# Performance work log

Hardware: AMD Instinct MI355X
Metric: run time of the kernel (lower is better)

The kernel has to match this reference:

```python
import jax, jax.numpy as jnp
import numpy as np

B, S, H = 1, 4096, 2048
NH, NKV, HD = 8, 4, 256
I = 8192
EPS = 1e-6
THETA = 10000.0
WINDOW = 4096  # hardcoded sliding window for even layer_idx
LAYER_IDX = 0


def rms_norm(x, w):
    v = jnp.mean(jnp.square(x), axis=-1, keepdims=True)
    return x * jax.lax.rsqrt(v + EPS) * w


def rotate_half(x):
    h = x.shape[-1] // 2
    return jnp.concatenate([-x[..., h:], x[..., :h]], axis=-1)


def apply_rope(q, k, positions):
    # q: [B,S,NH,HD], k: [B,S,NKV,HD], positions: [B,S]
    inv_freq = 1.0 / (THETA ** (jnp.arange(0, HD, 2, dtype=jnp.float32) / HD))
    freqs = positions.astype(jnp.float32)[..., None] * inv_freq  # [B,S,HD/2]
    emb = jnp.concatenate([freqs, freqs], axis=-1)               # [B,S,HD]
    cos = jnp.cos(emb)[:, :, None, :]
    sin = jnp.sin(emb)[:, :, None, :]
    q = q * cos + rotate_half(q) * sin
    k = k * cos + rotate_half(k) * sin
    return q, k


def forward(hidden_states, q_w, k_w, v_w, o_w, gate_w, up_w, down_w, ln1_w, ln2_w,
            attention_mask, position_ids):
    # ---- input RMSNorm + attention ----
    residual = hidden_states
    x = rms_norm(hidden_states, ln1_w)

    q = (x @ q_w).reshape(B, S, NH, HD)
    k = (x @ k_w).reshape(B, S, NKV, HD)
    v = (x @ v_w).reshape(B, S, NKV, HD)
    q, k = apply_rope(q, k, position_ids)

    # GQA: repeat kv heads to match query heads
    groups = NH // NKV
    k = jnp.repeat(k, groups, axis=2)  # [B,S,NH,HD]
    v = jnp.repeat(v, groups, axis=2)

    # masks: padding mask AND causal AND (even layer) local window of WINDOW
    row = jnp.arange(S)[:, None]
    col = jnp.arange(S)[None, :]
    causal = col <= row                                   # [S,S]
    combined = causal[None, None] & (attention_mask[:, None, None, :] > 0)
    if LAYER_IDX % 2 == 0:
        keep = ~(col <= row - WINDOW)                     # mask out keys older than WINDOW
        combined = combined & keep[None, None]
    neg = jnp.finfo(jnp.float32).min
    bias = jnp.where(combined, 0.0, neg).astype(jnp.float32)  # [B,1,S,S]

    scale = HD ** -0.5
    scores = jnp.einsum('bqhd,bkhd->bhqk', q, k) * scale + bias
    probs = jax.nn.softmax(scores, axis=-1)
    attn = jnp.einsum('bhqk,bkhd->bqhd', probs, v).reshape(B, S, NH * HD)
    attn_out = attn @ o_w

    hidden_states = residual + attn_out

    # ---- post-attention RMSNorm + gated-GeLU MLP ----
    residual = hidden_states
    x = rms_norm(hidden_states, ln2_w)
    mlp = (jax.nn.gelu(x @ gate_w, approximate=True) * (x @ up_w)) @ down_w
    return residual + mlp


def setup_inputs() -> dict:
    key = jax.random.key(0)
    ks = jax.random.split(key, 9)
    std = 0.02
    n = lambda k, shp: jax.random.normal(k, shp, dtype=jnp.float32) * std
    return {
        'hidden_states': jax.random.normal(ks[0], (B, S, H), dtype=jnp.float32),
        'q_w': n(ks[1], (H, NH * HD)),
        'k_w': n(ks[2], (H, NKV * HD)),
        'v_w': n(ks[3], (H, NKV * HD)),
        'o_w': n(ks[4], (NH * HD, H)),
        'gate_w': n(ks[5], (H, I)),
        'up_w': n(ks[6], (H, I)),
        'down_w': n(ks[7], (I, H)),
        'ln1_w': jnp.ones((H,), jnp.float32),
        'ln2_w': jnp.ones((H,), jnp.float32),
        'attention_mask': jnp.ones((B, S), jnp.int32),
        'position_ids': jnp.broadcast_to(jnp.arange(S, dtype=jnp.int32)[None, :], (B, S)),
    }


def reference(hidden_states, q_w, k_w, v_w, o_w, gate_w, up_w, down_w, ln1_w, ln2_w,
              attention_mask, position_ids):
    return forward(hidden_states, q_w, k_w, v_w, o_w, gate_w, up_w, down_w,
                   ln1_w, ln2_w, attention_mask, position_ids)
```

## Files before the change

### kernel.cpp

```cpp
#include <hip/hip_runtime.h>
#include <hip/hip_bf16.h>
#include <math.h>

#define S_LEN 4096
#define HID   2048
#define NHEADS 8
#define NKVH   4
#define HDIM   256
#define FFN    8192
#define WIN    4096

typedef __bf16 bf16_t;
typedef __bf16 bf16x4 __attribute__((ext_vector_type(4)));
typedef __bf16 bf16x8 __attribute__((ext_vector_type(8)));
typedef float  floatx4 __attribute__((ext_vector_type(4)));

__device__ inline float waveReduceSum(float v) {
#pragma unroll
    for (int o = 32; o > 0; o >>= 1) v += __shfl_xor(v, o);
    return v;
}
__device__ inline float blockReduceSum(float v, float* sh) {
    int tid = threadIdx.x;
    v = waveReduceSum(v);
    if ((tid & 63) == 0) sh[tid >> 6] = v;
    __syncthreads();
    v = sh[0] + sh[1] + sh[2] + sh[3];
    __syncthreads();
    return v;
}

template <typename T>
__global__ __launch_bounds__(256) void transpose_bf16_kernel(const T* __restrict__ in,
                                                             bf16_t* __restrict__ out,
                                                             int R, int C) {
    __shared__ float tile[32][33];
    int tx = threadIdx.x & 31;
    int ty = threadIdx.x >> 5;
    int c0 = blockIdx.x * 32;
    int r0 = blockIdx.y * 32;
#pragma unroll
    for (int i = 0; i < 4; ++i)
        tile[ty + i * 8][tx] = (float)in[(long long)(r0 + ty + i * 8) * C + c0 + tx];
    __syncthreads();
#pragma unroll
    for (int i = 0; i < 4; ++i)
        out[(long long)(c0 + ty + i * 8) * R + r0 + tx] = (bf16_t)tile[tx][ty + i * 8];
}

__global__ __launch_bounds__(256) void rmsnorm_kernel(const float* __restrict__ x,
                                                      const float* __restrict__ w,
                                                      bf16_t* __restrict__ out) {
    __shared__ float sh[4];
    int row = blockIdx.x;
    const float* xr = x + (long long)row * HID;
    float v[8];
    float ss = 0.f;
#pragma unroll
    for (int i = 0; i < 8; ++i) {
        v[i] = xr[threadIdx.x + i * 256];
        ss += v[i] * v[i];
    }
    ss = blockReduceSum(ss, sh);
    float sc = rsqrtf(ss * (1.0f / HID) + 1e-6f);
#pragma unroll
    for (int i = 0; i < 8; ++i) {
        int c = threadIdx.x + i * 256;
        out[(long long)row * HID + c] = (bf16_t)(v[i] * sc * w[c]);
    }
}

__global__ __launch_bounds__(256) void rope_kernel(bf16_t* __restrict__ q,
                                                   bf16_t* __restrict__ k,
                                                   const int* __restrict__ pos_ids) {
    int s = blockIdx.x;
    float p = (float)pos_ids[s];
    for (int t = threadIdx.x; t < (NHEADS + NKVH) * (HDIM / 2); t += 256) {
        int head = t >> 7;
        int i = t & 127;
        float inv = expf(-(2.0f * (float)i / (float)HDIM) * 9.210340371976184f);
        float f = p * inv;
        float sn, cs;
        sincosf(f, &sn, &cs);
        bf16_t* base = (head < NHEADS) ? (q + (long long)s * HID + head * HDIM)
                                       : (k + (long long)s * (NKVH * HDIM) + (head - NHEADS) * HDIM);
        float a = (float)base[i];
        float b = (float)base[i + 128];
        base[i]       = (bf16_t)(a * cs - b * sn);
        base[i + 128] = (bf16_t)(b * cs + a * sn);
    }
}

__global__ __launch_bounds__(256, 2) void flash_attn_kernel(const bf16_t* __restrict__ qg,
                                                            const bf16_t* __restrict__ kg,
                                                            const bf16_t* __restrict__ vTg,
                                                            bf16_t* __restrict__ op0,
                                                            bf16_t* __restrict__ opb123,
                                                            float* __restrict__ mlb,
                                                            const int* __restrict__ amask) {
    __shared__ bf16_t sK[64 * 256];
    __shared__ bf16_t sV[256 * 64];

    const int b = blockIdx.x;
    const int h = b & 7;
    const int j = b >> 3;
    const int jq = j & 3;
    const int pidx = j >> 2;
    const int tid = threadIdx.x;
    const int lane = tid & 63;
    const int w = tid >> 6;
    const int tl = lane & 15;
    const int quad = lane >> 4;

    const bf16_t* Qh = qg + h * HDIM;
    const bf16_t* Kh = kg + (h >> 1) * HDIM;
    const bf16_t* Vh = vTg + (long long)(h >> 1) * HDIM * S_LEN;
    bf16_t* Op = (jq == 0) ? op0 : opb123 + (long long)(jq - 1) * (S_LEN * HID);
    float* mlj = mlb + (long long)jq * (NHEADS * S_LEN * 2);
    bf16_t* sP = sK + w * (32 * 72);

#pragma unroll 1
    for (int half = 0; half < 2; ++half) {
        const int qi = half ? (31 - pidx) : pidx;
        const int qr0 = qi * 128;
        const int T = 2 * qi + 2;
        const int t0 = (T * jq) >> 2;
        const int t1 = (T * (jq + 1)) >> 2;
        const int irow = qr0 + w * 32 + tl;

        bf16x8 qf[2][8];
#pragma unroll
        for (int s = 0; s < 2; ++s) {
            const bf16_t* qrow = Qh + (long long)(irow + s * 16) * HID;
#pragma unroll
            for (int ks = 0; ks < 8; ++ks)
                qf[s][ks] = *(const bf16x8*)(qrow + (ks * 4 + quad) * 8);
        }

        floatx4 oacc[2][16] = {};
        float m_i[2] = {-3e38f, -3e38f};
        float l_i[2] = {0.f, 0.f};

        for (int t = t0; t < t1; ++t) {
            const int kt = t * 64;
#pragma unroll
            for (int it = 0; it < 8; ++it) {
                int f = it * 4 + w;
                {
                    int row = (f & 3) * 16 + tl;
                    int dc = (f >> 2) * 4 + quad;
                    const bf16_t* src = Kh + (long long)(kt + row) * (NKVH * HDIM) + dc * 8;
                    __builtin_amdgcn_global_load_lds((const __attribute__((address_space(1))) void*)src,
                                                     (__attribute__((address_space(3))) void*)(sK + (it * 256 + tid) * 8),
                                                     16, 0, 0);
                }
                {
                    int d = (f & 15) * 16 + tl;
                    int kc = (f >> 4) * 4 + quad;
                    const bf16_t* src = Vh + (long long)d * S_LEN + kt + kc * 8;
                    __builtin_amdgcn_global_load_lds((const __attribute__((address_space(1))) void*)src,
                                                     (__attribute__((address_space(3))) void*)(sV + (it * 256 + tid) * 8),
                                                     16, 0, 0);
                }
            }
            __builtin_amdgcn_s_waitcnt(0x0f70);
            __syncthreads();

            floatx4 sacc[2][4] = {};
#pragma unroll
            for (int ks = 0; ks < 8; ++ks) {
#pragma unroll
                for (int ni = 0; ni < 4; ++ni) {
                    bf16x8 kf = *(const bf16x8*)(sK + ((ks * 4 + ni) * 64 + lane) * 8);
                    sacc[0][ni] = __builtin_amdgcn_mfma_f32_16x16x32_bf16(kf, qf[0][ks], sacc[0][ni], 0, 0, 0);
                    sacc[1][ni] = __builtin_amdgcn_mfma_f32_16x16x32_bf16(kf, qf[1][ks], sacc[1][ni], 0, 0, 0);
                }
            }
            __syncthreads();

            int4 am4[4];
#pragma unroll
            for (int ni = 0; ni < 4; ++ni) am4[ni] = *(const int4*)(amask + kt + ni * 16 + quad * 4);
#pragma unroll
            for (int s = 0; s < 2; ++s) {
                const int ir = irow + s * 16;
                float sv[4][4];
                float mx = -3e38f;
#pragma unroll
                for (int ni = 0; ni < 4; ++ni) {
#pragma unroll
                    for (int r = 0; r < 4; ++r) {
                        int jk = kt + ni * 16 + quad * 4 + r;
                        int amr = (r == 0) ? am4[ni].x : (r == 1) ? am4[ni].y : (r == 2) ? am4[ni].z : am4[ni].w;
                        bool valid = (jk <= ir) && (jk > ir - WIN) && (amr > 0);
                        float x = valid ? sacc[s][ni][r] * 0.0625f : -3e38f;
                        sv[ni][r] = x;
                        mx = fmaxf(mx, x);
                    }
                }
                mx = fmaxf(mx, __shfl_xor(mx, 16));
                mx = fmaxf(mx, __shfl_xor(mx, 32));
                if (__any(mx > m_i[s])) {
                    float mnew = fmaxf(m_i[s], mx);
                    float alpha = __expf(m_i[s] - mnew);
                    m_i[s] = mnew;
                    l_i[s] *= alpha;
                    floatx4 av;
#pragma unroll
                    for (int r = 0; r < 4; ++r) av[r] = __shfl(alpha, quad * 4 + r);
#pragma unroll
                    for (int dt = 0; dt < 16; ++dt) oacc[s][dt] *= av;
                }
                float rs = 0.f;
#pragma unroll
                for (int ni = 0; ni < 4; ++ni) {
                    bf16x4 pk;
#pragma unroll
                    for (int r = 0; r < 4; ++r) {
                        float p = (sv[ni][r] > -1e37f) ? __expf(sv[ni][r] - m_i[s]) : 0.f;
                        rs += p;
                        pk[r] = (bf16_t)p;
                    }
                    *(bf16x4*)(sP + (s * 16 + tl) * 72 + ni * 16 + quad * 4) = pk;
                }
                rs += __shfl_xor(rs, 16);
                rs += __shfl_xor(rs, 32);
                l_i[s] += rs;
            }

#pragma unroll
            for (int k2 = 0; k2 < 2; ++k2) {
                bf16x8 pf0 = *(const bf16x8*)(sP + tl * 72 + k2 * 32 + quad * 8);
                bf16x8 pf1 = *(const bf16x8*)(sP + (16 + tl) * 72 + k2 * 32 + quad * 8);
#pragma unroll
                for (int dt = 0; dt < 16; ++dt) {
                    bf16x8 vf = *(const bf16x8*)(sV + ((k2 * 16 + dt) * 64 + lane) * 8);
                    oacc[0][dt] = __builtin_amdgcn_mfma_f32_16x16x32_bf16(pf0, vf, oacc[0][dt], 0, 0, 0);
                    oacc[1][dt] = __builtin_amdgcn_mfma_f32_16x16x32_bf16(pf1, vf, oacc[1][dt], 0, 0, 0);
                }
            }
            __syncthreads();
        }

#pragma unroll
        for (int s = 0; s < 2; ++s) {
            floatx4 inv;
#pragma unroll
            for (int r = 0; r < 4; ++r) {
                float lv = __shfl(l_i[s], quad * 4 + r);
                inv[r] = (lv > 0.f) ? 1.0f / lv : 0.f;
            }
#pragma unroll
            for (int dt = 0; dt < 16; ++dt) {
#pragma unroll
                for (int r = 0; r < 4; ++r) {
                    long long row = qr0 + w * 32 + s * 16 + quad * 4 + r;
                    Op[row * HID + h * HDIM + dt * 16 + tl] = (bf16_t)(oacc[s][dt][r] * inv[r]);
                }
            }
            if (quad == 0) {
                long long mi2 = ((long long)h * S_LEN + irow + s * 16) * 2;
                mlj[mi2] = m_i[s];
                mlj[mi2 + 1] = l_i[s];
            }
        }
    }
}

__global__ __launch_bounds__(256) void combine_kernel(const bf16_t* __restrict__ op0,
                                                      const bf16_t* __restrict__ opb123,
                                                      const float* __restrict__ mlb,
                                                      bf16_t* __restrict__ attnb) {
    int h = blockIdx.x;
    int row = blockIdx.y;
    int d = threadIdx.x;
    float m[4], l[4];
    float M = -3e38f;
#pragma unroll
    for (int j = 0; j < 4; ++j) {
        long long mi = (((long long)j * NHEADS + h) * S_LEN + row) * 2;
        m[j] = mlb[mi];
        l[j] = mlb[mi + 1];
        M = fmaxf(M, m[j]);
    }
    float wj[4], wsum = 0.f;
#pragma unroll
    for (int j = 0; j < 4; ++j) {
        wj[j] = (l[j] > 0.f) ? l[j] * __expf(m[j] - M) : 0.f;
        wsum += wj[j];
    }
    float inv = 1.0f / wsum;
    long long idx = (long long)row * HID + h * HDIM + d;
    float acc = wj[0] * (float)op0[idx];
#pragma unroll
    for (int j = 1; j < 4; ++j)
        acc += wj[j] * (float)opb123[(long long)(j - 1) * (S_LEN * HID) + idx];
    attnb[idx] = (bf16_t)(acc * inv);
}

template <int MODE>
__global__ __launch_bounds__(256) void gemm_kernel(const bf16_t* __restrict__ A, int lda,
                                                   const bf16_t* __restrict__ Bt, int ldb,
                                                   void* __restrict__ Cv, int ldc,
                                                   const void* __restrict__ aux, int K) {
    __shared__ bf16_t smem[2 * 128 * 64];
    bf16_t* sA = smem;
    bf16_t* sB = smem + 128 * 64;

    const int tid = threadIdx.x;
    const int n0 = blockIdx.x * 128;
    const int m0 = blockIdx.y * 128;

    const int lane = tid & 63;
    const int wid = tid >> 6;
    const int wm = (wid >> 1) * 64;
    const int wn = (wid & 1) * 64;
    const int tl = lane & 15;
    const int quad = lane >> 4;

    floatx4 acc[4][4] = {};

    for (int k0 = 0; k0 < K; k0 += 64) {
#pragma unroll
        for (int it = 0; it < 4; ++it) {
            int s = it * 256 + tid;
            int m = s >> 3;
            int sg = s & 7;
            int g = sg ^ (m & 7);
            const bf16_t* ga = A + (long long)(m0 + m) * lda + k0 + g * 8;
            __builtin_amdgcn_global_load_lds((const __attribute__((address_space(1))) void*)ga,
                                             (__attribute__((address_space(3))) void*)(sA + s * 8),
                                             16, 0, 0);
            const bf16_t* gb = Bt + (long long)(n0 + m) * ldb + k0 + g * 8;
            __builtin_amdgcn_global_load_lds((const __attribute__((address_space(1))) void*)gb,
                                             (__attribute__((address_space(3))) void*)(sB + s * 8),
                                             16, 0, 0);
        }
        __builtin_amdgcn_s_waitcnt(0x0f70);
        __syncthreads();

#pragma unroll
        for (int kk = 0; kk < 2; ++kk) {
            bf16x8 af[4], bfr[4];
#pragma unroll
            for (int mi = 0; mi < 4; ++mi) {
                int m = wm + mi * 16 + tl;
                int sg = (kk * 4 + quad) ^ (m & 7);
                af[mi] = *(const bf16x8*)(sA + m * 64 + sg * 8);
            }
#pragma unroll
            for (int ni = 0; ni < 4; ++ni) {
                int n = wn + ni * 16 + tl;
                int sg = (kk * 4 + quad) ^ (n & 7);
                bfr[ni] = *(const bf16x8*)(sB + n * 64 + sg * 8);
            }
#pragma unroll
            for (int mi = 0; mi < 4; ++mi)
#pragma unroll
                for (int ni = 0; ni < 4; ++ni)
                    acc[mi][ni] = __builtin_amdgcn_mfma_f32_16x16x32_bf16(af[mi], bfr[ni], acc[mi][ni], 0, 0, 0);
        }
        __syncthreads();
    }

#pragma unroll
    for (int mi = 0; mi < 4; ++mi) {
#pragma unroll
        for (int ni = 0; ni < 4; ++ni) {
#pragma unroll
            for (int r = 0; r < 4; ++r) {
                int gr = m0 + wm + mi * 16 + quad * 4 + r;
                int gc = n0 + wn + ni * 16 + tl;
                long long idx = (long long)gr * ldc + gc;
                float v = acc[mi][ni][r];
                if (MODE == 0) {
                    ((bf16_t*)Cv)[idx] = (bf16_t)v;
                } else if (MODE == 1) {
                    ((float*)Cv)[idx] = ((const float*)aux)[idx] + v;
                } else {
                    float g = (float)((const bf16_t*)aux)[idx];
                    float t = 0.7978845608028654f * (g + 0.044715f * g * g * g);
                    float ge = 0.5f * g * (1.0f + tanhf(t));
                    ((bf16_t*)Cv)[idx] = (bf16_t)(ge * v);
                }
            }
        }
    }
}

extern "C" void kernel_launch(void* const* d_in, const int* in_sizes, int n_in,
                              void* d_out, int out_size, void* d_ws, size_t ws_size,
                              hipStream_t stream) {
    const float* hidden = (const float*)d_in[0];
    const float* q_w    = (const float*)d_in[1];
    const float* k_w    = (const float*)d_in[2];
    const float* v_w    = (const float*)d_in[3];
    const float* o_w    = (const float*)d_in[4];
    const float* gate_w = (const float*)d_in[5];
    const float* up_w   = (const float*)d_in[6];
    const float* down_w = (const float*)d_in[7];
    const float* ln1_w  = (const float*)d_in[8];
    const float* ln2_w  = (const float*)d_in[9];
    const int* amask    = (const int*)d_in[10];
    const int* pos_ids  = (const int*)d_in[11];
    float* out = (float*)d_out;

    const size_t MB = 1ull << 20;
    char* ws = (char*)d_ws;
    bf16_t* wqT    = (bf16_t*)(ws + 0 * MB);
    bf16_t* wkT    = (bf16_t*)(ws + 8 * MB);
    bf16_t* wvT    = (bf16_t*)(ws + 12 * MB);
    bf16_t* woT    = (bf16_t*)(ws + 16 * MB);
    bf16_t* wgT    = (bf16_t*)(ws + 24 * MB);
    bf16_t* wuT    = (bf16_t*)(ws + 56 * MB);
    bf16_t* xb     = (bf16_t*)(ws + 88 * MB);
    bf16_t* qb     = (bf16_t*)(ws + 104 * MB);
    bf16_t* kb     = (bf16_t*)(ws + 120 * MB);
    bf16_t* vb     = (bf16_t*)(ws + 128 * MB);
    bf16_t* vT     = (bf16_t*)(ws + 136 * MB);
    bf16_t* op0    = (bf16_t*)(ws + 88 * MB);
    bf16_t* opb123 = (bf16_t*)(ws + 144 * MB);
    float*  mlb    = (float*) (ws + 192 * MB);
    bf16_t* attnb  = (bf16_t*)(ws + 104 * MB);
    bf16_t* xb2    = (bf16_t*)(ws + 120 * MB);
    bf16_t* wdT    = (bf16_t*)(ws + 144 * MB);
    bf16_t* gb     = (bf16_t*)(ws + 88 * MB);
    (void)ws_size; (void)in_sizes; (void)n_in; (void)out_size;

    dim3 blk(256);

    transpose_bf16_kernel<float><<<dim3(64, 64), blk, 0, stream>>>(q_w, wqT, 2048, 2048);
    transpose_bf16_kernel<float><<<dim3(32, 64), blk, 0, stream>>>(k_w, wkT, 2048, 1024);
    transpose_bf16_kernel<float><<<dim3(32, 64), blk, 0, stream>>>(v_w, wvT, 2048, 1024);
    transpose_bf16_kernel<float><<<dim3(64, 64), blk, 0, stream>>>(o_w, woT, 2048, 2048);
    transpose_bf16_kernel<float><<<dim3(256, 64), blk, 0, stream>>>(gate_w, wgT, 2048, 8192);
    transpose_bf16_kernel<float><<<dim3(256, 64), blk, 0, stream>>>(up_w, wuT, 2048, 8192);

    rmsnorm_kernel<<<dim3(S_LEN), blk, 0, stream>>>(hidden, ln1_w, xb);

    gemm_kernel<0><<<dim3(16, 32), blk, 0, stream>>>(xb, HID, wqT, HID, qb, 2048, nullptr, HID);
    gemm_kernel<0><<<dim3(8, 32), blk, 0, stream>>>(xb, HID, wkT, HID, kb, 1024, nullptr, HID);
    gemm_kernel<0><<<dim3(8, 32), blk, 0, stream>>>(xb, HID, wvT, HID, vb, 1024, nullptr, HID);

    rope_kernel<<<dim3(S_LEN), blk, 0, stream>>>(qb, kb, pos_ids);

    transpose_bf16_kernel<bf16_t><<<dim3(32, 128), blk, 0, stream>>>(vb, vT, S_LEN, 1024);

    flash_attn_kernel<<<dim3(512), blk, 0, stream>>>(qb, kb, vT, op0, opb123, mlb, amask);
    combine_kernel<<<dim3(NHEADS, S_LEN), blk, 0, stream>>>(op0, opb123, mlb, attnb);

    gemm_kernel<1><<<dim3(16, 32), blk, 0, stream>>>(attnb, 2048, woT, 2048, out, 2048, hidden, 2048);

    rmsnorm_kernel<<<dim3(S_LEN), blk, 0, stream>>>(out, ln2_w, xb2);

    transpose_bf16_kernel<float><<<dim3(64, 256), blk, 0, stream>>>(down_w, wdT, 8192, 2048);

    for (int c = 0; c < 2; ++c) {
        bf16_t* wgc = wgT + (size_t)c * 4096 * HID;
        bf16_t* wuc = wuT + (size_t)c * 4096 * HID;
        bf16_t* wdc = wdT + (size_t)c * 4096;
        gemm_kernel<0><<<dim3(32, 32), blk, 0, stream>>>(xb2, HID, wgc, HID, gb, 4096, nullptr, HID);
        gemm_kernel<2><<<dim3(32, 32), blk, 0, stream>>>(xb2, HID, wuc, HID, gb, 4096, gb, HID);
        gemm_kernel<1><<<dim3(16, 32), blk, 0, stream>>>(gb, 4096, wdc, FFN, out, 2048, out, 4096);
    }
}
```

Baseline: 1.393 ms.

## Share KV tiles across GQA head pair and double-buffer K loads in flash attention

Flash attention blocks now have 512 threads covering both query heads of a KV group, so each K/V tile loaded into LDS serves two heads. K tiles are double-buffered so the next tile's load overlaps the current tile's compute. The softmax scale is folded into the Q projection GEMM epilogue, and the causal check is skipped for tiles entirely below the diagonal. The window check is dropped because WIN equals S, so it never masks anything. LDS use grows and occupancy falls to one block per CU, and the combine kernel gains a guard against a zero weight sum.

```diff
diff --git a/kernel.cpp b/kernel.cpp
--- a/kernel.cpp
+++ b/kernel.cpp
@@ -91,42 +91,42 @@
     }
 }
 
-__global__ __launch_bounds__(256, 2) void flash_attn_kernel(const bf16_t* __restrict__ qg,
+__global__ __launch_bounds__(512, 1) void flash_attn_kernel(const bf16_t* __restrict__ qg,
                                                             const bf16_t* __restrict__ kg,
                                                             const bf16_t* __restrict__ vTg,
                                                             bf16_t* __restrict__ op0,
                                                             bf16_t* __restrict__ opb123,
                                                             float* __restrict__ mlb,
                                                             const int* __restrict__ amask) {
-    __shared__ bf16_t sK[64 * 256];
-    __shared__ bf16_t sV[256 * 64];
-
-    const int b = blockIdx.x;
-    const int h = b & 7;
-    const int j = b >> 3;
-    const int jq = j & 3;
-    const int pidx = j >> 2;
+    __shared__ bf16_t sK[2][64 * 256];
+    __shared__ bf16_t sV[64 * 256];
+    __shared__ bf16_t sPB[8 * 32 * 72];
+
+    const int kvh = blockIdx.y;
+    const int jq = blockIdx.z;
     const int tid = threadIdx.x;
     const int lane = tid & 63;
     const int w = tid >> 6;
+    const int wq = w & 3;
     const int tl = lane & 15;
     const int quad = lane >> 4;
+    const int h = kvh * 2 + (w >> 2);
 
     const bf16_t* Qh = qg + h * HDIM;
-    const bf16_t* Kh = kg + (h >> 1) * HDIM;
-    const bf16_t* Vh = vTg + (long long)(h >> 1) * HDIM * S_LEN;
+    const bf16_t* Kh = kg + kvh * HDIM;
+    const bf16_t* Vh = vTg + (long long)kvh * HDIM * S_LEN;
     bf16_t* Op = (jq == 0) ? op0 : opb123 + (long long)(jq - 1) * (S_LEN * HID);
     float* mlj = mlb + (long long)jq * (NHEADS * S_LEN * 2);
-    bf16_t* sP = sK + w * (32 * 72);
+    bf16_t* sP = sPB + w * (32 * 72);
 
 #pragma unroll 1
     for (int half = 0; half < 2; ++half) {
-        const int qi = half ? (31 - pidx) : pidx;
+        const int qi = half ? (31 - blockIdx.x) : blockIdx.x;
         const int qr0 = qi * 128;
         const int T = 2 * qi + 2;
         const int t0 = (T * jq) >> 2;
         const int t1 = (T * (jq + 1)) >> 2;
-        const int irow = qr0 + w * 32 + tl;
+        const int irow = qr0 + wq * 32 + tl;
 
         bf16x8 qf[2][8];
 #pragma unroll
@@ -141,105 +141,120 @@
         float m_i[2] = {-3e38f, -3e38f};
         float l_i[2] = {0.f, 0.f};
 
-        for (int t = t0; t < t1; ++t) {
-            const int kt = t * 64;
-#pragma unroll
-            for (int it = 0; it < 8; ++it) {
-                int f = it * 4 + w;
-                {
-                    int row = (f & 3) * 16 + tl;
-                    int dc = (f >> 2) * 4 + quad;
-                    const bf16_t* src = Kh + (long long)(kt + row) * (NKVH * HDIM) + dc * 8;
+        if (t0 < t1) {
+#pragma unroll
+            for (int it = 0; it < 4; ++it) {
+                int f = it * 8 + w;
+                const bf16_t* src = Kh + (long long)(t0 * 64 + (f & 3) * 16 + tl) * (NKVH * HDIM) + ((f >> 2) * 4 + quad) * 8;
+                __builtin_amdgcn_global_load_lds((const __attribute__((address_space(1))) void*)src,
+                                                 (__attribute__((address_space(3))) void*)(&sK[0][(it * 512 + tid) * 8]),
+                                                 16, 0, 0);
+            }
+            __syncthreads();
+            int cb = 0;
+#pragma unroll 1
+            for (int t = t0; t < t1; ++t) {
+                const int kt = t * 64;
+#pragma unroll
+                for (int it = 0; it < 4; ++it) {
+                    int f = it * 8 + w;
+                    const bf16_t* src = Vh + (long long)((f & 15) * 16 + tl) * S_LEN + kt + ((f >> 4) * 4 + quad) * 8;
                     __builtin_amdgcn_global_load_lds((const __attribute__((address_space(1))) void*)src,
-                                                     (__attribute__((address_space(3))) void*)(sK + (it * 256 + tid) * 8),
+                                                     (__attribute__((address_space(3))) void*)(&sV[(it * 512 + tid) * 8]),
                                                      16, 0, 0);
                 }
-                {
-                    int d = (f & 15) * 16 + tl;
-                    int kc = (f >> 4) * 4 + quad;
-                    const bf16_t* src = Vh + (long long)d * S_LEN + kt + kc * 8;
-                    __builtin_amdgcn_global_load_lds((const __attribute__((address_space(1))) void*)src,
-                                                     (__attribute__((address_space(3))) void*)(sV + (it * 256 + tid) * 8),
-                                                     16, 0, 0);
-                }
-            }
-            __builtin_amdgcn_s_waitcnt(0x0f70);
-            __syncthreads();
-
-            floatx4 sacc[2][4] = {};
-#pragma unroll
-            for (int ks = 0; ks < 8; ++ks) {
-#pragma unroll
-                for (int ni = 0; ni < 4; ++ni) {
-                    bf16x8 kf = *(const bf16x8*)(sK + ((ks * 4 + ni) * 64 + lane) * 8);
-                    sacc[0][ni] = __builtin_amdgcn_mfma_f32_16x16x32_bf16(kf, qf[0][ks], sacc[0][ni], 0, 0, 0);
-                    sacc[1][ni] = __builtin_amdgcn_mfma_f32_16x16x32_bf16(kf, qf[1][ks], sacc[1][ni], 0, 0, 0);
-                }
-            }
-            __syncthreads();
-
-            int4 am4[4];
-#pragma unroll
-            for (int ni = 0; ni < 4; ++ni) am4[ni] = *(const int4*)(amask + kt + ni * 16 + quad * 4);
-#pragma unroll
-            for (int s = 0; s < 2; ++s) {
-                const int ir = irow + s * 16;
-                float sv[4][4];
-                float mx = -3e38f;
-#pragma unroll
-                for (int ni = 0; ni < 4; ++ni) {
-#pragma unroll
-                    for (int r = 0; r < 4; ++r) {
-                        int jk = kt + ni * 16 + quad * 4 + r;
-                        int amr = (r == 0) ? am4[ni].x : (r == 1) ? am4[ni].y : (r == 2) ? am4[ni].z : am4[ni].w;
-                        bool valid = (jk <= ir) && (jk > ir - WIN) && (amr > 0);
-                        float x = valid ? sacc[s][ni][r] * 0.0625f : -3e38f;
-                        sv[ni][r] = x;
-                        mx = fmaxf(mx, x);
-                    }
-                }
-                mx = fmaxf(mx, __shfl_xor(mx, 16));
-                mx = fmaxf(mx, __shfl_xor(mx, 32));
-                if (__any(mx > m_i[s])) {
-                    float mnew = fmaxf(m_i[s], mx);
-                    float alpha = __expf(m_i[s] - mnew);
-                    m_i[s] = mnew;
-                    l_i[s] *= alpha;
-                    floatx4 av;
-#pragma unroll
-                    for (int r = 0; r < 4; ++r) av[r] = __shfl(alpha, quad * 4 + r);
-#pragma unroll
-                    for (int dt = 0; dt < 16; ++dt) oacc[s][dt] *= av;
-                }
-                float rs = 0.f;
-#pragma unroll
-                for (int ni = 0; ni < 4; ++ni) {
-                    bf16x4 pk;
-#pragma unroll
-                    for (int r = 0; r < 4; ++r) {
-                        float p = (sv[ni][r] > -1e37f) ? __expf(sv[ni][r] - m_i[s]) : 0.f;
-                        rs += p;
-                        pk[r] = (bf16_t)p;
-                    }
-                    *(bf16x4*)(sP + (s * 16 + tl) * 72 + ni * 16 + quad * 4) = pk;
-                }
-                rs += __shfl_xor(rs, 16);
-                rs += __shfl_xor(rs, 32);
-                l_i[s] += rs;
-            }
-
-#pragma unroll
-            for (int k2 = 0; k2 < 2; ++k2) {
-                bf16x8 pf0 = *(const bf16x8*)(sP + tl * 72 + k2 * 32 + quad * 8);
-                bf16x8 pf1 = *(const bf16x8*)(sP + (16 + tl) * 72 + k2 * 32 + quad * 8);
-#pragma unroll
-                for (int dt = 0; dt < 16; ++dt) {
-                    bf16x8 vf = *(const bf16x8*)(sV + ((k2 * 16 + dt) * 64 + lane) * 8);
-                    oacc[0][dt] = __builtin_amdgcn_mfma_f32_16x16x32_bf16(pf0, vf, oacc[0][dt], 0, 0, 0);
-                    oacc[1][dt] = __builtin_amdgcn_mfma_f32_16x16x32_bf16(pf1, vf, oacc[1][dt], 0, 0, 0);
-                }
-            }
-            __syncthreads();
+                if (t + 1 < t1) {
+#pragma unroll
+                    for (int it = 0; it < 4; ++it) {
+                        int f = it * 8 + w;
+                        const bf16_t* src = Kh + (long long)(kt + 64 + (f & 3) * 16 + tl) * (NKVH * HDIM) + ((f >> 2) * 4 + quad) * 8;
+                        __builtin_amdgcn_global_load_lds((const __attribute__((address_space(1))) void*)src,
+                                                         (__attribute__((address_space(3))) void*)(&sK[cb ^ 1][(it * 512 + tid) * 8]),
+                                                         16, 0, 0);
+                    }
+                }
+
+                const bf16_t* sKb = sK[cb];
+                floatx4 sacc[2][4] = {};
+#pragma unroll
+                for (int ks = 0; ks < 8; ++ks) {
+#pragma unroll
+                    for (int ni = 0; ni < 4; ++ni) {
+                        bf16x8 kf = *(const bf16x8*)(sKb + ((ks * 4 + ni) * 64 + lane) * 8);
+                        sacc[0][ni] = __builtin_amdgcn_mfma_f32_16x16x32_bf16(kf, qf[0][ks], sacc[0][ni], 0, 0, 0);
+                        sacc[1][ni] = __builtin_amdgcn_mfma_f32_16x16x32_bf16(kf, qf[1][ks], sacc[1][ni], 0, 0, 0);
+                    }
+                }
+                __syncthreads();
+
+                int4 am4[4];
+#pragma unroll
+                for (int ni = 0; ni < 4; ++ni) am4[ni] = *(const int4*)(amask + kt + ni * 16 + quad * 4);
+                const bool full = (kt + 64 <= qr0);
+#pragma unroll
+                for (int s = 0; s < 2; ++s) {
+                    const int ir = irow + s * 16;
+                    float sv[4][4];
+                    float mx = -3e38f;
+#pragma unroll
+                    for (int ni = 0; ni < 4; ++ni) {
+#pragma unroll
+                        for (int r = 0; r < 4; ++r) {
+                            int amr = (r == 0) ? am4[ni].x : (r == 1) ? am4[ni].y : (r == 2) ? am4[ni].z : am4[ni].w;
+                            bool valid = (amr > 0);
+                            if (!full) {
+                                int jk = kt + ni * 16 + quad * 4 + r;
+                                valid = valid && (jk <= ir);
+                            }
+                            float x = valid ? sacc[s][ni][r] : -3e38f;
+                            sv[ni][r] = x;
+                            mx = fmaxf(mx, x);
+                        }
+                    }
+                    mx = fmaxf(mx, __shfl_xor(mx, 16));
+                    mx = fmaxf(mx, __shfl_xor(mx, 32));
+                    if (__any(mx > m_i[s])) {
+                        float mnew = fmaxf(m_i[s], mx);
+                        float alpha = __expf(m_i[s] - mnew);
+                        m_i[s] = mnew;
+                        l_i[s] *= alpha;
+                        floatx4 av;
+#pragma unroll
+                        for (int r = 0; r < 4; ++r) av[r] = __shfl(alpha, quad * 4 + r);
+#pragma unroll
+                        for (int dt = 0; dt < 16; ++dt) oacc[s][dt] *= av;
+                    }
+                    float rs = 0.f;
+#pragma unroll
+                    for (int ni = 0; ni < 4; ++ni) {
+                        bf16x4 pk;
+#pragma unroll
+                        for (int r = 0; r < 4; ++r) {
+                            float p = (sv[ni][r] > -1e37f) ? __expf(sv[ni][r] - m_i[s]) : 0.f;
+                            rs += p;
+                            pk[r] = (bf16_t)p;
+                        }
+                        *(bf16x4*)(sP + (s * 16 + tl) * 72 + ni * 16 + quad * 4) = pk;
+                    }
+                    rs += __shfl_xor(rs, 16);
+                    rs += __shfl_xor(rs, 32);
+                    l_i[s] += rs;
+                }
+
+#pragma unroll
+                for (int k2 = 0; k2 < 2; ++k2) {
+                    bf16x8 pf0 = *(const bf16x8*)(sP + tl * 72 + k2 * 32 + quad * 8);
+                    bf16x8 pf1 = *(const bf16x8*)(sP + (16 + tl) * 72 + k2 * 32 + quad * 8);
+#pragma unroll
+                    for (int dt = 0; dt < 16; ++dt) {
+                        bf16x8 vf = *(const bf16x8*)(sV + ((k2 * 16 + dt) * 64 + lane) * 8);
+                        oacc[0][dt] = __builtin_amdgcn_mfma_f32_16x16x32_bf16(pf0, vf, oacc[0][dt], 0, 0, 0);
+                        oacc[1][dt] = __builtin_amdgcn_mfma_f32_16x16x32_bf16(pf1, vf, oacc[1][dt], 0, 0, 0);
+                    }
+                }
+                __syncthreads();
+                cb ^= 1;
+            }
         }
 
 #pragma unroll
@@ -254,7 +269,7 @@
             for (int dt = 0; dt < 16; ++dt) {
 #pragma unroll
                 for (int r = 0; r < 4; ++r) {
-                    long long row = qr0 + w * 32 + s * 16 + quad * 4 + r;
+                    long long row = qr0 + wq * 32 + s * 16 + quad * 4 + r;
                     Op[row * HID + h * HDIM + dt * 16 + tl] = (bf16_t)(oacc[s][dt][r] * inv[r]);
                 }
             }
@@ -289,7 +304,7 @@
         wj[j] = (l[j] > 0.f) ? l[j] * __expf(m[j] - M) : 0.f;
         wsum += wj[j];
     }
-    float inv = 1.0f / wsum;
+    float inv = (wsum > 0.f) ? 1.0f / wsum : 0.f;
     long long idx = (long long)row * HID + h * HDIM + d;
     float acc = wj[0] * (float)op0[idx];
 #pragma unroll
@@ -377,11 +392,13 @@
                     ((bf16_t*)Cv)[idx] = (bf16_t)v;
                 } else if (MODE == 1) {
                     ((float*)Cv)[idx] = ((const float*)aux)[idx] + v;
-                } else {
+                } else if (MODE == 2) {
                     float g = (float)((const bf16_t*)aux)[idx];
                     float t = 0.7978845608028654f * (g + 0.044715f * g * g * g);
                     float ge = 0.5f * g * (1.0f + tanhf(t));
                     ((bf16_t*)Cv)[idx] = (bf16_t)(ge * v);
+                } else {
+                    ((bf16_t*)Cv)[idx] = (bf16_t)(v * 0.0625f);
                 }
             }
         }
@@ -438,7 +455,7 @@
 
     rmsnorm_kernel<<<dim3(S_LEN), blk, 0, stream>>>(hidden, ln1_w, xb);
 
-    gemm_kernel<0><<<dim3(16, 32), blk, 0, stream>>>(xb, HID, wqT, HID, qb, 2048, nullptr, HID);
+    gemm_kernel<3><<<dim3(16, 32), blk, 0, stream>>>(xb, HID, wqT, HID, qb, 2048, nullptr, HID);
     gemm_kernel<0><<<dim3(8, 32), blk, 0, stream>>>(xb, HID, wkT, HID, kb, 1024, nullptr, HID);
     gemm_kernel<0><<<dim3(8, 32), blk, 0, stream>>>(xb, HID, wvT, HID, vb, 1024, nullptr, HID);
 
@@ -446,7 +463,7 @@
 
     transpose_bf16_kernel<bf16_t><<<dim3(32, 128), blk, 0, stream>>>(vb, vT, S_LEN, 1024);
 
-    flash_attn_kernel<<<dim3(512), blk, 0, stream>>>(qb, kb, vT, op0, opb123, mlb, amask);
+    flash_attn_kernel<<<dim3(16, NKVH, 4), dim3(512), 0, stream>>>(qb, kb, vT, op0, opb123, mlb, amask);
     combine_kernel<<<dim3(NHEADS, S_LEN), blk, 0, stream>>>(op0, opb123, mlb, attnb);
 
     gemm_kernel<1><<<dim3(16, 32), blk, 0, stream>>>(attnb, 2048, woT, 2048, out, 2048, hidden, 2048);
```

After: 1.354 ms. -2.8%, faster.
